# Optimization experiments

Hardware: AMD Instinct MI355X
Metric: run time of the kernel (lower is better)

The kernel has to match this reference:

```python
import jax, jax.numpy as jnp
import numpy as np

H = 2048          # hidden_size
NH = 16           # num_attention_heads
D = H // NH       # head dim = 128
FFN = 4 * H       # mlp hidden
EPS = 1e-5
NORM = float(np.sqrt(D))  # coeff=max(1,layer_number)=1 cancels in FusedScaleMaskSoftmax
NEG = -10000.0    # attention_mask_func fill value
L2EPS = 1e-12     # F.normalize eps


def layernorm(x, g, b):
    m = jnp.mean(x, axis=-1, keepdims=True)
    v = jnp.var(x, axis=-1, keepdims=True)
    return (x - m) * jax.lax.rsqrt(v + EPS) * g + b


def l2norm(x):
    n = jnp.sqrt(jnp.sum(x * x, axis=-1, keepdims=True))
    return x / jnp.maximum(n, L2EPS)


def mlp(x, w1, b1, w2, b2):
    # GPT MLP with skip_bias_add: returns (h@w2, bias)
    h = jax.nn.gelu(x @ w1 + b1, approximate=False)
    return h @ w2, b2


def setup_inputs():
    S, B, M = 2048, 2, 4096
    key = jax.random.key(0)
    ks = jax.random.split(key, 12)
    r = lambda i, shape: jax.random.normal(ks[i], shape, jnp.float32) * 0.02
    return {
        'x': jax.random.normal(ks[0], (S, B, H), jnp.float32),
        'past_hidden': jax.random.normal(ks[1], (M, B, H), jnp.float32),
        'mem_mask': jax.random.randint(ks[2], (B, 1, S, M), 0, 2) == 1,
        'ln1_g': jnp.ones((H,), jnp.float32), 'ln1_b': jnp.zeros((H,), jnp.float32),
        'ln2_g': jnp.ones((H,), jnp.float32), 'ln2_b': jnp.zeros((H,), jnp.float32),
        'ln3_g': jnp.ones((H,), jnp.float32), 'ln3_b': jnp.zeros((H,), jnp.float32),
        'mlp1_w1': r(3, (H, FFN)), 'mlp1_b1': jnp.zeros((FFN,), jnp.float32),
        'mlp1_w2': r(4, (FFN, H)), 'mlp1_b2': jnp.zeros((H,), jnp.float32),
        'mlp2_w1': r(5, (H, FFN)), 'mlp2_b1': jnp.zeros((FFN,), jnp.float32),
        'mlp2_w2': r(6, (FFN, H)), 'mlp2_b2': jnp.zeros((H,), jnp.float32),
        'wq': r(7, (H, H)), 'bq': jnp.zeros((H,), jnp.float32),
        'wkv': r(8, (H, 2 * H)), 'bkv': jnp.zeros((2 * H,), jnp.float32),
        'wd': r(9, (H, H)), 'bd': jnp.zeros((H,), jnp.float32),
    }


def reference(x, past_hidden, mem_mask, ln1_g, ln1_b, ln2_g, ln2_b, ln3_g, ln3_b,
              mlp1_w1, mlp1_b1, mlp1_w2, mlp1_b2, mlp2_w1, mlp2_b1, mlp2_w2, mlp2_b2,
              wq, bq, wkv, bkv, wd, bd):
    S, B, _ = x.shape
    M = past_hidden.shape[0]

    # mlp1 branch (output replaces x, residual is NOT added for mlp1 per source)
    o1, bias1 = mlp(layernorm(x, ln1_g, ln1_b), mlp1_w1, mlp1_b1, mlp1_w2, mlp1_b2)
    x = o1 + bias1

    # memory attention
    h = layernorm(x, ln2_g, ln2_b)
    q = l2norm((h @ wq + bq).reshape(S, B, NH, D))            # [S,B,NH,D]
    kv = (past_hidden @ wkv + bkv).reshape(M, B, NH, 2 * D)   # [M,B,NH,2D]
    k = l2norm(kv[..., :D])
    v = l2norm(kv[..., D:])
    scores = jnp.einsum('sbhd,mbhd->bhsm', q, k) / NORM       # [B,NH,S,M]
    scores = jnp.where(mem_mask, NEG, scores.astype(jnp.float32))
    probs = jax.nn.softmax(scores, axis=-1).astype(q.dtype)
    ctx = jnp.einsum('bhsm,mbhd->sbhd', probs, v).reshape(S, B, H)
    x = x + ctx @ wd + bd

    # mlp2 branch with residual
    o2, bias2 = mlp(layernorm(x, ln3_g, ln3_b), mlp2_w1, mlp2_b1, mlp2_w2, mlp2_b2)
    return x + o2 + bias2
```

## Files before the change

kernel.cpp:

```cpp
#include <hip/hip_runtime.h>


typedef unsigned short ushort_t;
typedef __attribute__((ext_vector_type(8))) short bf16x8;
typedef __attribute__((ext_vector_type(4))) float f32x4;

#define DEVI __device__ __forceinline__

DEVI ushort_t f2bf(float f) {
  unsigned int u = __builtin_bit_cast(unsigned int, f);
  u += 0x7FFFu + ((u >> 16) & 1u);
  return (ushort_t)(u >> 16);
}
DEVI float bf2f(ushort_t h) {
  unsigned int u = ((unsigned int)h) << 16;
  return __builtin_bit_cast(float, u);
}

DEVI void load_lds16(const void* g, void* l) {
  __builtin_amdgcn_global_load_lds(
      (__attribute__((address_space(1))) void*)(g),
      (__attribute__((address_space(3))) void*)(l), 16, 0, 0);
}

__global__ void detect_mask_k(const unsigned int* __restrict__ m, int* __restrict__ flag) {
  unsigned int v = m[threadIdx.x];
  unsigned long long ok = __ballot(v <= 1u);
  if (threadIdx.x == 0) *flag = (ok == ~0ull) ? 1 : 0;
}

__global__ __launch_bounds__(256)
void mask_pack_k(const void* __restrict__ maskp, const int* __restrict__ mtype,
                 unsigned long long* __restrict__ out, int nwords) {
  const int mint = *mtype;
  const int lane = threadIdx.x & 63;
  const int wglob = blockIdx.x * 4 + (threadIdx.x >> 6);
  const int nw = gridDim.x * 4;
  const unsigned char* m8 = (const unsigned char*)maskp;
  const int* m32 = (const int*)maskp;
  for (int i = wglob; i < nwords; i += nw) {
    const size_t e = (size_t)i * 64 + lane;
    const bool v = mint ? (m32[e] != 0) : (m8[e] != 0);
    unsigned long long bits = __ballot(v);
    if (lane == 0) out[i] = bits;
  }
}

__global__ __launch_bounds__(256)
void transpose_w(const float* __restrict__ in, ushort_t* __restrict__ out, int K, int N) {
  __shared__ float t[64][65];
  const int tid = threadIdx.x;
  const int tx = tid & 63, ty = tid >> 6;
  const int n0 = blockIdx.x * 64, k0 = blockIdx.y * 64;
#pragma unroll
  for (int i = 0; i < 16; ++i)
    t[ty + i * 4][tx] = in[(size_t)(k0 + ty + i * 4) * N + n0 + tx];
  __syncthreads();
  const int l32 = tid & 31, nr = tid >> 5;
#pragma unroll
  for (int i = 0; i < 8; ++i) {
    const int n = nr + i * 8;
    ushort2 o;
    o.x = f2bf(t[2 * l32][n]);
    o.y = f2bf(t[2 * l32 + 1][n]);
    *(ushort2*)&out[(size_t)(n0 + n) * K + k0 + 2 * l32] = o;
  }
}

__global__ void f32_to_bf16_k(const float* __restrict__ in, ushort_t* __restrict__ out, int n4) {
  int i = blockIdx.x * blockDim.x + threadIdx.x;
  int stride = gridDim.x * blockDim.x;
  for (; i < n4; i += stride) {
    float4 v = ((const float4*)in)[i];
    ushort4 o;
    o.x = f2bf(v.x); o.y = f2bf(v.y); o.z = f2bf(v.z); o.w = f2bf(v.w);
    ((ushort4*)out)[i] = o;
  }
}

__global__ __launch_bounds__(256)
void ln_kernel(const float* __restrict__ in, const float* __restrict__ gam,
               const float* __restrict__ bet, ushort_t* __restrict__ out) {
  const int row = blockIdx.x;
  const float* p = in + (size_t)row * 2048;
  const int tid = threadIdx.x;
  float4 v0 = ((const float4*)p)[tid * 2];
  float4 v1 = ((const float4*)p)[tid * 2 + 1];
  float s = v0.x + v0.y + v0.z + v0.w + v1.x + v1.y + v1.z + v1.w;
  float q = v0.x * v0.x + v0.y * v0.y + v0.z * v0.z + v0.w * v0.w +
            v1.x * v1.x + v1.y * v1.y + v1.z * v1.z + v1.w * v1.w;
#pragma unroll
  for (int m = 1; m < 64; m <<= 1) { s += __shfl_xor(s, m); q += __shfl_xor(q, m); }
  __shared__ float red[8];
  const int w = tid >> 6;
  if ((tid & 63) == 0) { red[w] = s; red[4 + w] = q; }
  __syncthreads();
  s = red[0] + red[1] + red[2] + red[3];
  q = red[4] + red[5] + red[6] + red[7];
  const float mean = s * (1.f / 2048.f);
  const float var = q * (1.f / 2048.f) - mean * mean;
  const float rs = rsqrtf(var + 1e-5f);
  float4 g0 = ((const float4*)gam)[tid * 2], g1 = ((const float4*)gam)[tid * 2 + 1];
  float4 b0 = ((const float4*)bet)[tid * 2], b1 = ((const float4*)bet)[tid * 2 + 1];
  ushort4 o0, o1;
  o0.x = f2bf((v0.x - mean) * rs * g0.x + b0.x);
  o0.y = f2bf((v0.y - mean) * rs * g0.y + b0.y);
  o0.z = f2bf((v0.z - mean) * rs * g0.z + b0.z);
  o0.w = f2bf((v0.w - mean) * rs * g0.w + b0.w);
  o1.x = f2bf((v1.x - mean) * rs * g1.x + b1.x);
  o1.y = f2bf((v1.y - mean) * rs * g1.y + b1.y);
  o1.z = f2bf((v1.z - mean) * rs * g1.z + b1.z);
  o1.w = f2bf((v1.w - mean) * rs * g1.w + b1.w);
  ushort4* ob = (ushort4*)(out + (size_t)row * 2048);
  ob[tid * 2] = o0;
  ob[tid * 2 + 1] = o1;
}

__global__ __launch_bounds__(256)
void vtrans_k(const ushort_t* __restrict__ kv, ushort_t* __restrict__ vt) {
  __shared__ ushort_t t[32][33];
  const int tx = threadIdx.x, ty = threadIdx.y;
  const int m0 = blockIdx.x * 32, d0 = blockIdx.y * 32, bh = blockIdx.z;
  const int b = bh >> 4, h = bh & 15;
#pragma unroll
  for (int i = 0; i < 4; ++i)
    t[ty + i * 8][tx] = kv[((size_t)(m0 + ty + i * 8) * 2 + b) * 4096 + h * 256 + 128 + d0 + tx];
  __syncthreads();
#pragma unroll
  for (int i = 0; i < 4; ++i)
    vt[((size_t)bh * 128 + d0 + ty + i * 8) * 4096 + m0 + tx] = t[tx][ty + i * 8];
}

template <int EPI>
__global__ __launch_bounds__(256, 3)
void gemm_s(const ushort_t* __restrict__ A, const ushort_t* __restrict__ Bt,
            const float* __restrict__ bias, const float* __restrict__ Xres,
            void* __restrict__ Out, int N, int K, int GM, float nscale) {
  __shared__ ushort_t lA[128 * 64];
  __shared__ ushort_t lB[128 * 64];

  const int tid = threadIdx.x;
  const int lane = tid & 63;
  const int w = tid >> 6;
  const int l15 = lane & 15, lhi = lane >> 4;
  const int wr = w >> 1, wc = w & 1;

  const int nwg = gridDim.x;
  const int cpx = nwg >> 3;
  const int swz = (blockIdx.x & 7) * cpx + (blockIdx.x >> 3);
  const int tm = swz % GM, tn = swz / GM;

  size_t aSrc[4], bSrc[4];
#pragma unroll
  for (int i = 0; i < 4; ++i) {
    const int ch = i * 256 + tid;
    const int row = ch >> 3;
    const int colb = ((ch & 7) * 16) ^ ((row & 7) << 4);
    aSrc[i] = (size_t)(tm * 128 + row) * K + (colb >> 1);
    bSrc[i] = (size_t)(tn * 128 + row) * K + (colb >> 1);
  }

  f32x4 acc[4][4] = {};

  const int KT = K >> 6;
  for (int kt = 0; kt < KT; ++kt) {
    const int k0 = kt << 6;
#pragma unroll
    for (int i = 0; i < 4; ++i) {
      load_lds16(A + aSrc[i] + k0, (char*)lA + (i * 256 + tid) * 16);
      load_lds16(Bt + bSrc[i] + k0, (char*)lB + (i * 256 + tid) * 16);
    }
    __syncthreads();
#pragma unroll
    for (int kk = 0; kk < 2; ++kk) {
      const int kb = kk * 64 + lhi * 16;
      bf16x8 bfr[4], af[4];
#pragma unroll
      for (int nf = 0; nf < 4; ++nf) {
        const int rb = wc * 64 + nf * 16 + l15;
        bfr[nf] = *(const bf16x8*)((const char*)lB + rb * 128 + (kb ^ ((rb & 7) << 4)));
      }
#pragma unroll
      for (int mf = 0; mf < 4; ++mf) {
        const int ra = wr * 64 + mf * 16 + l15;
        af[mf] = *(const bf16x8*)((const char*)lA + ra * 128 + (kb ^ ((ra & 7) << 4)));
      }
#pragma unroll
      for (int mf = 0; mf < 4; ++mf)
#pragma unroll
        for (int nf = 0; nf < 4; ++nf)
          acc[mf][nf] = __builtin_amdgcn_mfma_f32_16x16x32_bf16(af[mf], bfr[nf], acc[mf][nf], 0, 0, 0);
    }
    __syncthreads();
  }

  const int row0 = tm * 128 + wr * 64;
  const int col0 = tn * 128 + wc * 64;
  float bj[4];
#pragma unroll
  for (int nf = 0; nf < 4; ++nf) bj[nf] = bias[col0 + nf * 16 + l15];

  float inv_n[4][4];
  if constexpr (EPI == 4) {
    float part[4][4];
#pragma unroll
    for (int mf = 0; mf < 4; ++mf)
#pragma unroll
      for (int r = 0; r < 4; ++r) {
        float p = 0.f;
#pragma unroll
        for (int nf = 0; nf < 4; ++nf) {
          const float v = acc[mf][nf][r] + bj[nf];
          p += v * v;
        }
        part[mf][r] = p;
      }
#pragma unroll
    for (int ms = 1; ms < 16; ms <<= 1)
#pragma unroll
      for (int mf = 0; mf < 4; ++mf)
#pragma unroll
        for (int r = 0; r < 4; ++r) part[mf][r] += __shfl_xor(part[mf][r], ms);
    float* sq = (float*)lA;
    if (l15 == 0) {
#pragma unroll
      for (int mf = 0; mf < 4; ++mf)
#pragma unroll
        for (int r = 0; r < 4; ++r)
          sq[wc * 128 + wr * 64 + mf * 16 + lhi * 4 + r] = part[mf][r];
    }
    __syncthreads();
#pragma unroll
    for (int mf = 0; mf < 4; ++mf)
#pragma unroll
      for (int r = 0; r < 4; ++r) {
        const int idx = wr * 64 + mf * 16 + lhi * 4 + r;
        const float tot = sq[idx] + sq[128 + idx];
        inv_n[mf][r] = nscale / fmaxf(sqrtf(tot), 1e-12f);
      }
  }

#pragma unroll
  for (int mf = 0; mf < 4; ++mf) {
#pragma unroll
    for (int nf = 0; nf < 4; ++nf) {
      const int col = col0 + nf * 16 + l15;
#pragma unroll
      for (int r = 0; r < 4; ++r) {
        const int row = row0 + mf * 16 + lhi * 4 + r;
        const size_t idx = (size_t)row * N + col;
        float v = acc[mf][nf][r] + bj[nf];
        if constexpr (EPI == 0) {
          v = 0.5f * v * (1.f + erff(v * 0.70710678118654752f));
          ((ushort_t*)Out)[idx] = f2bf(v);
        } else if constexpr (EPI == 2) {
          ((float*)Out)[idx] = v;
        } else if constexpr (EPI == 3) {
          ((float*)Out)[idx] = Xres[idx] + v;
        } else {
          ((ushort_t*)Out)[idx] = f2bf(v * inv_n[mf][r]);
        }
      }
    }
  }
}

template <int EPI>
__global__ __launch_bounds__(512, 4)
void gemm_w(const ushort_t* __restrict__ A, const ushort_t* __restrict__ Bt,
            const float* __restrict__ bias, void* __restrict__ Out,
            int N, int K, int GM, float nscale) {
  __shared__ ushort_t lA[128 * 64];
  __shared__ ushort_t lB[256 * 64];

  const int tid = threadIdx.x;
  const int lane = tid & 63;
  const int w = tid >> 6;
  const int l15 = lane & 15, lhi = lane >> 4;
  const int wr = w >> 2, wc = w & 3;

  const int nwg = gridDim.x;
  const int cpx = nwg >> 3;
  const int swz = (blockIdx.x & 7) * cpx + (blockIdx.x >> 3);
  const int tm = swz % GM, tn = swz / GM;

  size_t aSrc[2], bSrc[4];
#pragma unroll
  for (int i = 0; i < 2; ++i) {
    const int ch = i * 512 + tid;
    const int row = ch >> 3;
    const int colb = ((ch & 7) * 16) ^ ((row & 7) << 4);
    aSrc[i] = (size_t)(tm * 128 + row) * K + (colb >> 1);
  }
#pragma unroll
  for (int i = 0; i < 4; ++i) {
    const int ch = i * 512 + tid;
    const int row = ch >> 3;
    const int colb = ((ch & 7) * 16) ^ ((row & 7) << 4);
    bSrc[i] = (size_t)(tn * 256 + row) * K + (colb >> 1);
  }

  f32x4 acc[4][4] = {};

  const int KT = K >> 6;
  for (int kt = 0; kt < KT; ++kt) {
    const int k0 = kt << 6;
#pragma unroll
    for (int i = 0; i < 2; ++i)
      load_lds16(A + aSrc[i] + k0, (char*)lA + (i * 512 + tid) * 16);
#pragma unroll
    for (int i = 0; i < 4; ++i)
      load_lds16(Bt + bSrc[i] + k0, (char*)lB + (i * 512 + tid) * 16);
    __syncthreads();
#pragma unroll
    for (int kk = 0; kk < 2; ++kk) {
      const int kb = kk * 64 + lhi * 16;
      bf16x8 bfr[4], af[4];
#pragma unroll
      for (int nf = 0; nf < 4; ++nf) {
        const int rb = wc * 64 + nf * 16 + l15;
        bfr[nf] = *(const bf16x8*)((const char*)lB + rb * 128 + (kb ^ ((rb & 7) << 4)));
      }
#pragma unroll
      for (int mf = 0; mf < 4; ++mf) {
        const int ra = wr * 64 + mf * 16 + l15;
        af[mf] = *(const bf16x8*)((const char*)lA + ra * 128 + (kb ^ ((ra & 7) << 4)));
      }
#pragma unroll
      for (int mf = 0; mf < 4; ++mf)
#pragma unroll
        for (int nf = 0; nf < 4; ++nf)
          acc[mf][nf] = __builtin_amdgcn_mfma_f32_16x16x32_bf16(af[mf], bfr[nf], acc[mf][nf], 0, 0, 0);
    }
    __syncthreads();
  }

  const int row0 = tm * 128 + wr * 64;
  const int col0 = tn * 256 + wc * 64;
  float bj[4];
#pragma unroll
  for (int nf = 0; nf < 4; ++nf) bj[nf] = bias[col0 + nf * 16 + l15];

  float inv_n[4][4];
  if constexpr (EPI == 4) {
    float part[4][4];
#pragma unroll
    for (int mf = 0; mf < 4; ++mf)
#pragma unroll
      for (int r = 0; r < 4; ++r) {
        float p = 0.f;
#pragma unroll
        for (int nf = 0; nf < 4; ++nf) {
          const float v = acc[mf][nf][r] + bj[nf];
          p += v * v;
        }
        part[mf][r] = p;
      }
#pragma unroll
    for (int ms = 1; ms < 16; ms <<= 1)
#pragma unroll
      for (int mf = 0; mf < 4; ++mf)
#pragma unroll
        for (int r = 0; r < 4; ++r) part[mf][r] += __shfl_xor(part[mf][r], ms);
    float* sq = (float*)lA;
    if (l15 == 0) {
#pragma unroll
      for (int mf = 0; mf < 4; ++mf)
#pragma unroll
        for (int r = 0; r < 4; ++r)
          sq[wc * 128 + wr * 64 + mf * 16 + lhi * 4 + r] = part[mf][r];
    }
    __syncthreads();
#pragma unroll
    for (int mf = 0; mf < 4; ++mf)
#pragma unroll
      for (int r = 0; r < 4; ++r) {
        const int idx = wr * 64 + mf * 16 + lhi * 4 + r;
        const float tot = sq[wc * 128 + idx] + sq[(wc ^ 1) * 128 + idx];
        inv_n[mf][r] = nscale / fmaxf(sqrtf(tot), 1e-12f);
      }
  }

#pragma unroll
  for (int mf = 0; mf < 4; ++mf) {
#pragma unroll
    for (int nf = 0; nf < 4; ++nf) {
      const int col = col0 + nf * 16 + l15;
#pragma unroll
      for (int r = 0; r < 4; ++r) {
        const int row = row0 + mf * 16 + lhi * 4 + r;
        const size_t idx = (size_t)row * N + col;
        float v = acc[mf][nf][r] + bj[nf];
        if constexpr (EPI == 0) {
          v = 0.5f * v * (1.f + erff(v * 0.70710678118654752f));
          ((ushort_t*)Out)[idx] = f2bf(v);
        } else {
          ((ushort_t*)Out)[idx] = f2bf(v * inv_n[mf][r]);
        }
      }
    }
  }
}

__global__ __launch_bounds__(512, 4)
void attn_k(const ushort_t* __restrict__ Q, const ushort_t* __restrict__ KV,
            const ushort_t* __restrict__ VT,
            const unsigned long long* __restrict__ PM,
            ushort_t* __restrict__ CTX) {
  __shared__ ushort_t lk[2][64 * 128];
  __shared__ ushort_t lvt[2][128 * 64];
  __shared__ ushort_t lp[8][16 * 64];

  const int tid = threadIdx.x, lane = tid & 63, w = tid >> 6;
  const int l15 = lane & 15, lhi = lane >> 4;
  const int wid = ((blockIdx.x & 7) << 6) + (blockIdx.x >> 3);
  const int qt = wid & 15, pair = wid >> 4;
  const int b = pair >> 4, h = pair & 15;

  size_t kSrc[2], vSrc[2];
  int kDst[2], vDst[2];
#pragma unroll
  for (int i = 0; i < 2; ++i) {
    const int ch = (i * 8 + w) * 64 + lane;
    {
      const int row = ch >> 4;
      const int cb = ((ch & 15) * 16) ^ ((row & 7) << 4);
      kSrc[i] = ((size_t)row * 2 + b) * 4096 + h * 256 + (cb >> 1);
      kDst[i] = (i * 8 + w) * 1024;
    }
    {
      const int row = ch >> 3;
      const int cb = ((ch & 7) * 16) ^ ((row & 7) << 4);
      vSrc[i] = (size_t)pair * 128 * 4096 + (size_t)row * 4096 + (cb >> 1);
      vDst[i] = (i * 8 + w) * 1024;
    }
  }

  bf16x8 aq[4];
  {
    const ushort_t* qbase =
        Q + ((size_t)(qt * 128 + w * 16 + l15) * 2 + b) * 2048 + h * 128 + lhi * 8;
#pragma unroll
    for (int kk = 0; kk < 4; ++kk) aq[kk] = *(const bf16x8*)(qbase + kk * 32);
  }

  float l_acc[4] = {0.f, 0.f, 0.f, 0.f};
  f32x4 acc_o[8] = {};
  const unsigned long long* mrow =
      PM + (size_t)(b * 2048 + qt * 128 + w * 16 + lhi * 4) * 64;
  const int l15p16 = l15 + 16;

#pragma unroll
  for (int i = 0; i < 2; ++i) {
    load_lds16(KV + kSrc[i], (char*)lk[0] + kDst[i]);
    load_lds16(VT + vSrc[i], (char*)lvt[0] + vDst[i]);
  }
  __syncthreads();

  int cur = 0;
  for (int t = 0; t < 64; ++t) {
    if (t < 63) {
      const size_t kAdd = (size_t)(t + 1) * 64 * 8192;
      const int vAdd = (t + 1) * 64;
#pragma unroll
      for (int i = 0; i < 2; ++i) {
        load_lds16(KV + kSrc[i] + kAdd, (char*)lk[cur ^ 1] + kDst[i]);
        load_lds16(VT + vSrc[i] + vAdd, (char*)lvt[cur ^ 1] + vDst[i]);
      }
    }
    unsigned long long mw[4];
#pragma unroll
    for (int r = 0; r < 4; ++r) mw[r] = mrow[r * 64 + t];

    f32x4 sa[4] = {};
#pragma unroll
    for (int kk = 0; kk < 4; ++kk) {
#pragma unroll
      for (int j = 0; j < 4; ++j) {
        const int krow = j * 16 + l15;
        const int bcb = (kk * 64 + lhi * 16) ^ ((krow & 7) << 4);
        bf16x8 bk = *(const bf16x8*)((const char*)lk[cur] + krow * 256 + bcb);
        sa[j] = __builtin_amdgcn_mfma_f32_16x16x32_bf16(aq[kk], bk, sa[j], 0, 0, 0);
      }
    }

#pragma unroll
    for (int r = 0; r < 4; ++r) {
      const unsigned int mlo = (unsigned int)mw[r];
      const unsigned int mhi = (unsigned int)(mw[r] >> 32);
#pragma unroll
      for (int j = 0; j < 4; ++j) {
        const unsigned int sel = (j < 2) ? mlo : mhi;
        const int sh = (j & 1) ? l15p16 : l15;
        const bool mk = (sel >> sh) & 1u;
        const float p = __expf(sa[j][r]);
        const float pv = mk ? 0.f : p;
        sa[j][r] = pv;
        l_acc[r] += pv;
      }
    }

#pragma unroll
    for (int r = 0; r < 4; ++r) {
      unsigned int pk0, pk1;
      asm("v_cvt_pk_bf16_f32 %0, %1, %2" : "=v"(pk0) : "v"(sa[0][r]), "v"(sa[1][r]));
      asm("v_cvt_pk_bf16_f32 %0, %1, %2" : "=v"(pk1) : "v"(sa[2][r]), "v"(sa[3][r]));
      const int prow = lhi * 4 + r;
      char* base = (char*)lp[w] + prow * 128;
      const int swz = (prow & 7) << 4;
      *(ushort_t*)(base + ((l15 * 2) ^ swz)) = (ushort_t)pk0;
      *(ushort_t*)(base + (((16 + l15) * 2) ^ swz)) = (ushort_t)(pk0 >> 16);
      *(ushort_t*)(base + (((32 + l15) * 2) ^ swz)) = (ushort_t)pk1;
      *(ushort_t*)(base + (((48 + l15) * 2) ^ swz)) = (ushort_t)(pk1 >> 16);
    }

#pragma unroll
    for (int ks = 0; ks < 2; ++ks) {
      const int acb2 = (ks * 64 + lhi * 16) ^ ((l15 & 7) << 4);
      bf16x8 ap = *(const bf16x8*)((const char*)lp[w] + l15 * 128 + acb2);
#pragma unroll
      for (int d = 0; d < 8; ++d) {
        const int vrow = d * 16 + l15;
        const int vcb = (ks * 64 + lhi * 16) ^ ((vrow & 7) << 4);
        bf16x8 bv = *(const bf16x8*)((const char*)lvt[cur] + vrow * 128 + vcb);
        acc_o[d] = __builtin_amdgcn_mfma_f32_16x16x32_bf16(ap, bv, acc_o[d], 0, 0, 0);
      }
    }
    __syncthreads();
    cur ^= 1;
  }

#pragma unroll
  for (int ms = 1; ms < 16; ms <<= 1)
#pragma unroll
    for (int r = 0; r < 4; ++r) l_acc[r] += __shfl_xor(l_acc[r], ms);

#pragma unroll
  for (int r = 0; r < 4; ++r) {
    const float inv = 1.f / fmaxf(l_acc[r], 1e-20f);
    const size_t orow = ((size_t)(qt * 128 + w * 16 + lhi * 4 + r) * 2 + b) * 2048 + h * 128;
#pragma unroll
    for (int d = 0; d < 8; ++d)
      CTX[orow + d * 16 + l15] = f2bf(acc_o[d][r] * inv);
  }
}

extern "C" void kernel_launch(void* const* d_in, const int* in_sizes, int n_in,
                              void* d_out, int out_size, void* d_ws, size_t ws_size,
                              hipStream_t stream) {
  (void)in_sizes; (void)n_in; (void)out_size; (void)ws_size;
  const float* x    = (const float*)d_in[0];
  const float* ph   = (const float*)d_in[1];
  const void*  mask = d_in[2];
  const float* ln1g = (const float*)d_in[3];
  const float* ln1b = (const float*)d_in[4];
  const float* ln2g = (const float*)d_in[5];
  const float* ln2b = (const float*)d_in[6];
  const float* ln3g = (const float*)d_in[7];
  const float* ln3b = (const float*)d_in[8];
  const float* w1a  = (const float*)d_in[9];
  const float* b1a  = (const float*)d_in[10];
  const float* w2a  = (const float*)d_in[11];
  const float* b2a  = (const float*)d_in[12];
  const float* w1b  = (const float*)d_in[13];
  const float* b1b  = (const float*)d_in[14];
  const float* w2b  = (const float*)d_in[15];
  const float* b2b  = (const float*)d_in[16];
  const float* wq   = (const float*)d_in[17];
  const float* bq   = (const float*)d_in[18];
  const float* wkv  = (const float*)d_in[19];
  const float* bkv  = (const float*)d_in[20];
  const float* wd   = (const float*)d_in[21];
  const float* bd   = (const float*)d_in[22];

  char* ws = (char*)d_ws;
  int* flag = (int*)ws;
  size_t off = 256;
  auto alloc = [&](size_t bytes) {
    void* p = ws + off;
    off += (bytes + 255) & ~(size_t)255;
    return p;
  };
  ushort_t* WT1   = (ushort_t*)alloc(2048ull * 8192 * 2);
  ushort_t* WT2   = (ushort_t*)alloc(2048ull * 8192 * 2);
  ushort_t* WQT   = (ushort_t*)alloc(2048ull * 2048 * 2);
  ushort_t* WKVT  = (ushort_t*)alloc(2048ull * 4096 * 2);
  ushort_t* WDT   = (ushort_t*)alloc(2048ull * 2048 * 2);
  ushort_t* H1    = (ushort_t*)alloc(4096ull * 2048 * 2);
  ushort_t* GELU  = (ushort_t*)alloc(4096ull * 8192 * 2);
  float*    X     = (float*)alloc(4096ull * 2048 * 4);
  ushort_t* QRAW  = (ushort_t*)alloc(4096ull * 2048 * 2);
  ushort_t* PH16  = (ushort_t*)alloc(8192ull * 2048 * 2);
  ushort_t* KVRAW = (ushort_t*)alloc(8192ull * 4096 * 2);
  ushort_t* VT    = PH16;
  ushort_t* CTX   = WKVT;
  unsigned long long* PMASK = (unsigned long long*)GELU;

  const dim3 tb(32, 8);
  const float SSCALE = 0.088388347648318447f;

  detect_mask_k<<<1, 64, 0, stream>>>((const unsigned int*)mask, flag);

  transpose_w<<<dim3(128, 32), 256, 0, stream>>>(w1a, WT1, 2048, 8192);
  transpose_w<<<dim3(32, 128), 256, 0, stream>>>(w2a, WT2, 8192, 2048);
  transpose_w<<<dim3(32, 32), 256, 0, stream>>>(wq, WQT, 2048, 2048);
  transpose_w<<<dim3(64, 32), 256, 0, stream>>>(wkv, WKVT, 2048, 4096);
  transpose_w<<<dim3(32, 32), 256, 0, stream>>>(wd, WDT, 2048, 2048);

  ln_kernel<<<4096, 256, 0, stream>>>(x, ln1g, ln1b, H1);
  gemm_w<0><<<1024, 512, 0, stream>>>(H1, WT1, b1a, GELU, 8192, 2048, 32, 0.f);
  gemm_s<2><<<512, 256, 0, stream>>>(GELU, WT2, b2a, nullptr, X, 2048, 8192, 32, 0.f);

  mask_pack_k<<<1024, 256, 0, stream>>>(mask, flag, PMASK, 262144);

  ln_kernel<<<4096, 256, 0, stream>>>(X, ln2g, ln2b, H1);
  gemm_s<4><<<512, 256, 0, stream>>>(H1, WQT, bq, nullptr, QRAW, 2048, 2048, 32, SSCALE);
  f32_to_bf16_k<<<2048, 256, 0, stream>>>(ph, PH16, 8192 * 2048 / 4);
  gemm_w<4><<<1024, 512, 0, stream>>>(PH16, WKVT, bkv, KVRAW, 4096, 2048, 64, 1.0f);
  vtrans_k<<<dim3(128, 4, 32), tb, 0, stream>>>(KVRAW, VT);
  attn_k<<<512, 512, 0, stream>>>(QRAW, KVRAW, VT, PMASK, CTX);
  gemm_s<3><<<512, 256, 0, stream>>>(CTX, WDT, bd, X, X, 2048, 2048, 32, 0.f);

  ln_kernel<<<4096, 256, 0, stream>>>(X, ln3g, ln3b, H1);
  transpose_w<<<dim3(128, 32), 256, 0, stream>>>(w1b, WT1, 2048, 8192);
  transpose_w<<<dim3(32, 128), 256, 0, stream>>>(w2b, WT2, 8192, 2048);
  gemm_w<0><<<1024, 512, 0, stream>>>(H1, WT1, b1b, GELU, 8192, 2048, 32, 0.f);
  gemm_s<3><<<512, 256, 0, stream>>>(GELU, WT2, b2b, X, d_out, 2048, 8192, 32, 0.f);
}
```

Baseline: 1.270 ms.

## Split-K the MLP down-projection GEMMs with a separate reduction kernel

Replaces the two 4096x2048x8192 down-projection GEMMs with a split-K variant. It splits K into two halves across 1024 workgroups that write fp32 partials into the KVRAW buffer, then runs an elementwise reduction kernel that adds the two partials, the bias and optionally the residual. The aim is more parallelism and better occupancy than the 512-workgroup gemm_s launch on a large-K problem. The cost is extra global traffic, writing and re-reading two 32MB fp32 partial buffers, plus an extra kernel launch per GEMM.

```diff
diff --git a/kernel.cpp b/kernel.cpp
--- a/kernel.cpp
+++ b/kernel.cpp
@@ -262,6 +262,113 @@
         }
       }
     }
+  }
+}
+
+__global__ __launch_bounds__(256, 3)
+void gemm_sk(const ushort_t* __restrict__ A, const ushort_t* __restrict__ Bt,
+             float* __restrict__ Part, int N, int Kslice, int LDK, int GM,
+             size_t pstride) {
+  __shared__ ushort_t lA[128 * 64];
+  __shared__ ushort_t lB[128 * 64];
+
+  const int tid = threadIdx.x;
+  const int lane = tid & 63;
+  const int w = tid >> 6;
+  const int l15 = lane & 15, lhi = lane >> 4;
+  const int wr = w >> 1, wc = w & 1;
+
+  const int nwg = gridDim.x;
+  const int cpx = nwg >> 3;
+  const int swz = (blockIdx.x & 7) * cpx + (blockIdx.x >> 3);
+  const int ks = swz & 1;
+  const int tile = swz >> 1;
+  const int tm = tile % GM, tn = tile / GM;
+
+  const ushort_t* Ab = A + (size_t)ks * Kslice;
+  const ushort_t* Bb = Bt + (size_t)ks * Kslice;
+
+  size_t aSrc[4], bSrc[4];
+#pragma unroll
+  for (int i = 0; i < 4; ++i) {
+    const int ch = i * 256 + tid;
+    const int row = ch >> 3;
+    const int colb = ((ch & 7) * 16) ^ ((row & 7) << 4);
+    aSrc[i] = (size_t)(tm * 128 + row) * LDK + (colb >> 1);
+    bSrc[i] = (size_t)(tn * 128 + row) * LDK + (colb >> 1);
+  }
+
+  f32x4 acc[4][4] = {};
+
+  const int KT = Kslice >> 6;
+  for (int kt = 0; kt < KT; ++kt) {
+    const int k0 = kt << 6;
+#pragma unroll
+    for (int i = 0; i < 4; ++i) {
+      load_lds16(Ab + aSrc[i] + k0, (char*)lA + (i * 256 + tid) * 16);
+      load_lds16(Bb + bSrc[i] + k0, (char*)lB + (i * 256 + tid) * 16);
+    }
+    __syncthreads();
+#pragma unroll
+    for (int kk = 0; kk < 2; ++kk) {
+      const int kb = kk * 64 + lhi * 16;
+      bf16x8 bfr[4], af[4];
+#pragma unroll
+      for (int nf = 0; nf < 4; ++nf) {
+        const int rb = wc * 64 + nf * 16 + l15;
+        bfr[nf] = *(const bf16x8*)((const char*)lB + rb * 128 + (kb ^ ((rb & 7) << 4)));
+      }
+#pragma unroll
+      for (int mf = 0; mf < 4; ++mf) {
+        const int ra = wr * 64 + mf * 16 + l15;
+        af[mf] = *(const bf16x8*)((const char*)lA + ra * 128 + (kb ^ ((ra & 7) << 4)));
+      }
+#pragma unroll
+      for (int mf = 0; mf < 4; ++mf)
+#pragma unroll
+        for (int nf = 0; nf < 4; ++nf)
+          acc[mf][nf] = __builtin_amdgcn_mfma_f32_16x16x32_bf16(af[mf], bfr[nf], acc[mf][nf], 0, 0, 0);
+    }
+    __syncthreads();
+  }
+
+  const int row0 = tm * 128 + wr * 64;
+  const int col0 = tn * 128 + wc * 64;
+  float* outp = Part + (size_t)ks * pstride;
+#pragma unroll
+  for (int mf = 0; mf < 4; ++mf)
+#pragma unroll
+    for (int nf = 0; nf < 4; ++nf) {
+      const int col = col0 + nf * 16 + l15;
+#pragma unroll
+      for (int r = 0; r < 4; ++r) {
+        const int row = row0 + mf * 16 + lhi * 4 + r;
+        outp[(size_t)row * N + col] = acc[mf][nf][r];
+      }
+    }
+}
+
+template <int WITH_RES>
+__global__ __launch_bounds__(256)
+void redk(const float* __restrict__ P, const float* __restrict__ bias,
+          const float* __restrict__ Xres, float* __restrict__ out,
+          int n4, int pstride4) {
+  int i = blockIdx.x * 256 + threadIdx.x;
+  const int stride = gridDim.x * 256;
+  for (; i < n4; i += stride) {
+    float4 a = ((const float4*)P)[i];
+    float4 b = ((const float4*)P)[i + pstride4];
+    float4 bv = ((const float4*)bias)[i & 511];
+    float4 r;
+    r.x = a.x + b.x + bv.x;
+    r.y = a.y + b.y + bv.y;
+    r.z = a.z + b.z + bv.z;
+    r.w = a.w + b.w + bv.w;
+    if constexpr (WITH_RES) {
+      float4 xr = ((const float4*)Xres)[i];
+      r.x += xr.x; r.y += xr.y; r.z += xr.z; r.w += xr.w;
+    }
+    ((float4*)out)[i] = r;
   }
 }
 
@@ -595,9 +702,11 @@
   ushort_t* VT    = PH16;
   ushort_t* CTX   = WKVT;
   unsigned long long* PMASK = (unsigned long long*)GELU;
+  float* PART = (float*)KVRAW;
 
   const dim3 tb(32, 8);
   const float SSCALE = 0.088388347648318447f;
+  const size_t PSTRIDE = 4096ull * 2048;
 
   detect_mask_k<<<1, 64, 0, stream>>>((const unsigned int*)mask, flag);
 
@@ -609,7 +718,8 @@
 
   ln_kernel<<<4096, 256, 0, stream>>>(x, ln1g, ln1b, H1);
   gemm_w<0><<<1024, 512, 0, stream>>>(H1, WT1, b1a, GELU, 8192, 2048, 32, 0.f);
-  gemm_s<2><<<512, 256, 0, stream>>>(GELU, WT2, b2a, nullptr, X, 2048, 8192, 32, 0.f);
+  gemm_sk<<<1024, 256, 0, stream>>>(GELU, WT2, PART, 2048, 4096, 8192, 32, PSTRIDE);
+  redk<0><<<2048, 256, 0, stream>>>(PART, b2a, nullptr, X, 2097152, (int)(PSTRIDE / 4));
 
   mask_pack_k<<<1024, 256, 0, stream>>>(mask, flag, PMASK, 262144);
 
@@ -625,5 +735,6 @@
   transpose_w<<<dim3(128, 32), 256, 0, stream>>>(w1b, WT1, 2048, 8192);
   transpose_w<<<dim3(32, 128), 256, 0, stream>>>(w2b, WT2, 8192, 2048);
   gemm_w<0><<<1024, 512, 0, stream>>>(H1, WT1, b1b, GELU, 8192, 2048, 32, 0.f);
-  gemm_s<3><<<512, 256, 0, stream>>>(GELU, WT2, b2b, X, d_out, 2048, 8192, 32, 0.f);
-}
+  gemm_sk<<<1024, 256, 0, stream>>>(GELU, WT2, PART, 2048, 4096, 8192, 32, PSTRIDE);
+  redk<1><<<2048, 256, 0, stream>>>(PART, b2b, X, (float*)d_out, 2097152, (int)(PSTRIDE / 4));
+}
```

After: 1.329 ms. 4.6% more time.
